# Kernel optimization log

Hardware: AMD Instinct MI355X
Metric: run time of the kernel (lower is better)

Reference implementation:

```python
import jax, jax.numpy as jnp
import numpy as np

N = 100000
E = 1600000
NEG_SLOPE_ATTN = 0.2   # DGL GATConv default negative_slope
NEG_SLOPE_ACT = 0.01   # F.leaky_relu default


def gat_conv(x, src, dst, W, al, ar, b):
    """DGL-style GATConv with a single head.
    x: [N, Fin]; W: [Fin, H*Fout]; al, ar: [H, Fout]; b: [H*Fout].
    Returns [N, H, Fout]."""
    H, Fout = al.shape
    h = (x @ W).reshape(-1, H, Fout)                 # [N,H,Fout]
    el = jnp.sum(h * al, axis=-1)                    # [N,H]
    er = jnp.sum(h * ar, axis=-1)                    # [N,H]
    e = jax.nn.leaky_relu(el[src] + er[dst], NEG_SLOPE_ATTN)  # [E,H]
    # edge softmax over incoming edges of each dst node
    m = jax.ops.segment_max(e, dst, num_segments=N)  # [N,H]
    ex = jnp.exp(e - m[dst])                         # [E,H]
    denom = jax.ops.segment_sum(ex, dst, num_segments=N)      # [N,H]
    a = ex / denom[dst]                              # [E,H]
    msg = h[src] * a[:, :, None]                     # [E,H,Fout]
    out = jax.ops.segment_sum(msg, dst, num_segments=N)       # [N,H,Fout]
    return out + b.reshape(1, H, Fout)


def setup_inputs() -> dict:
    key = jax.random.key(0)
    ks = jax.random.split(key, 16)
    features = jax.random.normal(ks[0], (N, 3), dtype=jnp.float32)
    src = jax.random.randint(ks[1], (E,), 0, N)
    dst = jax.random.randint(ks[2], (E,), 0, N)

    def glorot(k, shape):
        fan = shape[0] + shape[-1]
        s = jnp.sqrt(2.0 / fan).astype(jnp.float32)
        return jax.random.normal(k, shape, dtype=jnp.float32) * s

    W1 = glorot(ks[3], (3, 64));   al1 = glorot(ks[4], (1, 64));  ar1 = glorot(ks[5], (1, 64));  b1 = jnp.zeros((64,), jnp.float32)
    W2 = glorot(ks[6], (64, 64));  al2 = glorot(ks[7], (1, 64));  ar2 = glorot(ks[8], (1, 64));  b2 = jnp.zeros((64,), jnp.float32)
    W3 = glorot(ks[9], (64, 3));   al3 = glorot(ks[10], (1, 3));  ar3 = glorot(ks[11], (1, 3));  b3 = jnp.zeros((3,), jnp.float32)
    return {"features": features, "src": src, "dst": dst,
            "W1": W1, "al1": al1, "ar1": ar1, "b1": b1,
            "W2": W2, "al2": al2, "ar2": ar2, "b2": b2,
            "W3": W3, "al3": al3, "ar3": ar3, "b3": b3}


def reference(features, src, dst, W1, al1, ar1, b1, W2, al2, ar2, b2, W3, al3, ar3, b3):
    x = gat_conv(features, src, dst, W1, al1, ar1, b1)      # [N,1,64]
    x = jax.nn.leaky_relu(x, NEG_SLOPE_ACT)
    x = gat_conv(x[:, 0, :], src, dst, W2, al2, ar2, b2)     # [N,1,64]
    x = jax.nn.leaky_relu(x, NEG_SLOPE_ACT)
    x = gat_conv(x[:, 0, :], src, dst, W3, al3, ar3, b3)     # [N,1,3]
    return x[:, 0, :]                                        # [N,3]
```

## Files before the change

### kernel.cpp

```cpp
#include <hip/hip_runtime.h>
#include <hip/hip_fp16.h>
#include <math.h>


#define NEG_BIG (-1e30f)
#define SORT_CAP 6144
#define SLOT 64
#define CHUNK 8192

__device__ inline float waveSum(float v) {
#pragma unroll
  for (int off = 32; off; off >>= 1) v += __shfl_xor(v, off, 64);
  return v;
}

__device__ inline float halfSum(float v) {
#pragma unroll
  for (int off = 16; off; off >>= 1) v += __shfl_xor(v, off, 64);
  return v;
}

__device__ inline float halfMax(float v) {
#pragma unroll
  for (int off = 16; off; off >>= 1) v = fmaxf(v, __shfl_xor(v, off, 64));
  return v;
}

__device__ inline int waveMaxI(int v) {
#pragma unroll
  for (int off = 32; off; off >>= 1) v = max(v, __shfl_xor(v, off, 64));
  return v;
}

__device__ inline int rlI(int v, int l) { return __builtin_amdgcn_readlane(v, l); }
__device__ inline float rlF(float v, int l) {
  return __int_as_float(__builtin_amdgcn_readlane(__float_as_int(v), l));
}
__device__ inline int ntI(const int* p) { return __builtin_nontemporal_load(p); }

__global__ __launch_bounds__(1024) void k_binpad(
    const int* __restrict__ src, const int* __restrict__ dst,
    unsigned* __restrict__ binned, int* __restrict__ cnts,
    const float* __restrict__ x, const float* __restrict__ W1,
    const float* __restrict__ al1, const float* __restrict__ ar1,
    float4* __restrict__ x4, float* __restrict__ er1,
    int E, int N, int NBK, int NCH, int CB) {
  __shared__ int lcnt[512];
  __shared__ float su[6];
  int tid = threadIdx.x;
  if ((int)blockIdx.x < CB) {
    int c = blockIdx.x;
    for (int b = tid; b < NBK; b += 1024) lcnt[b] = 0;
    __syncthreads();
    int e0 = c * CHUNK;
    int e1 = min(e0 + CHUNK, E);
    for (int e = e0 + tid; e < e1; e += 1024) {
      int dd = ntI(&dst[e]);
      int ss = ntI(&src[e]);
      int b = dd >> 8;
      int pos = atomicAdd(&lcnt[b], 1);
      if (pos < SLOT)
        binned[((size_t)b * NCH + c) * SLOT + pos] =
            ((unsigned)(dd & 255) << 24) | (unsigned)ss;
    }
    __syncthreads();
    for (int b = tid; b < NBK; b += 1024)
      cnts[(size_t)c * NBK + b] = min(lcnt[b], SLOT);
  } else {
    if (tid < 64) {
      float a = al1[tid], r = ar1[tid];
#pragma unroll
      for (int i = 0; i < 3; ++i) {
        float w = W1[i * 64 + tid];
        float ui = waveSum(w * a);
        float vi = waveSum(w * r);
        if (tid == 0) { su[i] = ui; su[3 + i] = vi; }
      }
    }
    __syncthreads();
    int n = ((int)blockIdx.x - CB) * 1024 + tid;
    if (n >= N) return;
    float x0 = __builtin_nontemporal_load(&x[n * 3]);
    float x1 = __builtin_nontemporal_load(&x[n * 3 + 1]);
    float x2 = __builtin_nontemporal_load(&x[n * 3 + 2]);
    float el = fmaf(x0, su[0], fmaf(x1, su[1], x2 * su[2]));
    float er = fmaf(x0, su[3], fmaf(x1, su[4], x2 * su[5]));
    x4[n] = make_float4(x0, x1, x2, el);
    er1[n] = er;
  }
}

__global__ __launch_bounds__(256) void k_sort(
    const unsigned* __restrict__ binned, const int* __restrict__ cnts,
    int* __restrict__ csr, int* __restrict__ startv, int* __restrict__ degs,
    int N, int NBK, int NCH) {
  __shared__ unsigned sbuf[SORT_CAP];
  __shared__ unsigned obuf[SORT_CAP];
  __shared__ int hist[256];
  __shared__ int scn[256];
  __shared__ int cur[256];
  __shared__ int csc[256];
  int b = blockIdx.x;
  int tid = threadIdx.x;
  int total = 0;
  for (int cb = 0; cb < NCH; cb += 256) {
    int c = cb + tid;
    int v = (c < NCH) ? cnts[(size_t)c * NBK + b] : 0;
    csc[tid] = v;
    __syncthreads();
    for (int off = 1; off < 256; off <<= 1) {
      int u = (tid >= off) ? csc[tid - off] : 0;
      __syncthreads();
      csc[tid] += u;
      __syncthreads();
    }
    int dbase = total + csc[tid] - v;
    if (c < NCH && v > 0) {
      const unsigned* rs = binned + ((size_t)b * NCH + c) * SLOT;
      for (int i = 0; i < v; ++i) {
        int di = dbase + i;
        if (di < SORT_CAP) sbuf[di] = rs[i];
      }
    }
    total += csc[255];
    __syncthreads();
  }
  int cnt = min(total, SORT_CAP);
  int gbase = b * SORT_CAP;
  hist[tid] = 0;
  __syncthreads();
  for (int i = tid; i < cnt; i += 256) atomicAdd(&hist[sbuf[i] >> 24], 1);
  __syncthreads();
  int v = hist[tid];
  scn[tid] = v;
  __syncthreads();
  for (int off = 1; off < 256; off <<= 1) {
    int u = (tid >= off) ? scn[tid - off] : 0;
    __syncthreads();
    scn[tid] += u;
    __syncthreads();
  }
  int excl = scn[tid] - v;
  cur[tid] = excl;
  int dn = b * 256 + tid;
  if (dn < N) { startv[dn] = gbase + excl; degs[dn] = v; }
  __syncthreads();
  for (int i = tid; i < cnt; i += 256) {
    unsigned w = sbuf[i];
    int p = atomicAdd(&cur[w >> 24], 1);
    obuf[p] = w & 0xFFFFFFu;
  }
  __syncthreads();
  for (int i = tid; i < cnt; i += 256) csr[gbase + i] = (int)obuf[i];
}

__global__ __launch_bounds__(128) void k_agg1x(
    const float4* __restrict__ x4, const float* __restrict__ er1,
    const float* __restrict__ W1, const float* __restrict__ b1,
    const float* __restrict__ W2, const float* __restrict__ al2,
    const float* __restrict__ ar2, const int* __restrict__ start,
    const int* __restrict__ degs, const int* __restrict__ csr,
    float4* __restrict__ a4, float* __restrict__ er2, int N) {
  __shared__ float4 sWp[64];
  __shared__ float2 sLR[64];
  int tid = threadIdx.x;
  if (tid < 64) {
    sWp[tid] = make_float4(W1[tid], W1[64 + tid], W1[128 + tid], b1[tid]);
    float sa = 0.f, sr = 0.f;
#pragma unroll 8
    for (int f = 0; f < 64; ++f) {
      float w = W2[tid * 64 + f];
      sa = fmaf(w, al2[f], sa);
      sr = fmaf(w, ar2[f], sr);
    }
    sLR[tid] = make_float2(sa, sr);
  }
  __syncthreads();
  int n = blockIdx.x * 128 + tid;
  if (n >= N) return;
  int beg = start[n];
  int end = beg + degs[n];
  float ern = er1[n];
  float m = NEG_BIG, d = 0.f, X0 = 0.f, X1 = 0.f, X2 = 0.f;
  int s0, s1, s2, s3;
  float4 h0, h1, h2, h3v;
  s0 = (beg + 0 < end) ? ntI(&csr[beg + 0]) : 0;
  s0 = ((unsigned)s0 < (unsigned)N) ? s0 : 0; h0 = x4[s0];
  s1 = (beg + 1 < end) ? ntI(&csr[beg + 1]) : 0;
  s1 = ((unsigned)s1 < (unsigned)N) ? s1 : 0; h1 = x4[s1];
  s2 = (beg + 2 < end) ? ntI(&csr[beg + 2]) : 0;
  s2 = ((unsigned)s2 < (unsigned)N) ? s2 : 0; h2 = x4[s2];
  s3 = (beg + 3 < end) ? ntI(&csr[beg + 3]) : 0;
  s3 = ((unsigned)s3 < (unsigned)N) ? s3 : 0; h3v = x4[s3];
  for (int i = beg; i < end; ++i) {
    float4 hv = h0;
    h0 = h1; h1 = h2; h2 = h3v;
    int ip = i + 4;
    int sp = (ip < end) ? ntI(&csr[ip]) : 0;
    sp = ((unsigned)sp < (unsigned)N) ? sp : 0;
    h3v = x4[sp];
    float e = hv.w + ern;
    e = e > 0.f ? e : 0.2f * e;
    float mn = fmaxf(m, e);
    float sc = __expf(m - mn);
    float q = __expf(e - mn);
    d = fmaf(d, sc, q);
    X0 = fmaf(X0, sc, q * hv.x);
    X1 = fmaf(X1, sc, q * hv.y);
    X2 = fmaf(X2, sc, q * hv.z);
    m = mn;
  }
  float inv = (end > beg) ? 1.f / d : 0.f;
  float A0 = X0 * inv, A1 = X1 * inv, A2 = X2 * inv;
  float el = 0.f, er = 0.f;
#pragma unroll 4
  for (int k = 0; k < 64; ++k) {
    float4 w = sWp[k];
    float v = fmaf(A2, w.z, fmaf(A1, w.y, fmaf(A0, w.x, w.w)));
    v = v > 0.f ? v : 0.01f * v;
    float2 lr = sLR[k];
    el = fmaf(v, lr.x, el);
    er = fmaf(v, lr.y, er);
  }
  a4[n] = make_float4(A0, A1, A2, el);
  er2[n] = er;
}

__global__ __launch_bounds__(64) void k_agg2r(
    const float4* __restrict__ a4, const float* __restrict__ er2,
    const int* __restrict__ start, const int* __restrict__ degs,
    const int* __restrict__ csr, const float* __restrict__ W1,
    const float* __restrict__ b1, __half* __restrict__ xa, int N) {
  __shared__ float4 sAV[64];
  int tid = threadIdx.x;
  int lane = tid & 63, hl = lane & 31, half = lane >> 5;
  int pn = blockIdx.x * 2 + half;
  int n = (pn < N) ? pn : 0;
  int beg = start[n];
  int deg = degs[n];
  int end = beg + deg;
  int maxd = __builtin_amdgcn_readfirstlane(waveMaxI(deg));
  float ern = er2[n];
  int k0 = 2 * hl;
  float wa0 = W1[k0],     wb0 = W1[64 + k0],     wc0 = W1[128 + k0],     bb0 = b1[k0];
  float wa1 = W1[k0 + 1], wb1 = W1[64 + k0 + 1], wc1 = W1[128 + k0 + 1], bb1 = b1[k0 + 1];
  float acc0 = 0.f, acc1 = 0.f;

  float aA = 0.f, v0s = 0.f, v1s = 0.f, v2s = 0.f;
  if (maxd <= 32) {
    int idx = beg + hl;
    int s = (idx < end) ? ntI(&csr[idx]) : 0;
    s = ((unsigned)s < (unsigned)N) ? s : 0;
    float4 av = a4[s];
    float e = av.w + ern;
    e = e > 0.f ? e : 0.2f * e;
    e = (idx < end) ? e : NEG_BIG;
    float mm = halfMax(e);
    float q = __expf(e - mm);
    float dsum = halfSum(q);
    float inv = (deg > 0) ? 1.f / dsum : 0.f;
    aA = q * inv;
    v0s = av.x; v1s = av.y; v2s = av.z;
  }
  sAV[half * 32 + hl] = make_float4(aA, v0s, v1s, v2s);
  __syncthreads();

  if (maxd <= 32) {
    const float4* sp = &sAV[half * 32];
    for (int j = 0; j < maxd; j += 4) {
#pragma unroll
      for (int k = 0; k < 4; ++k) {
        float4 w = sp[j + k];
        float a = w.x;
        float v0 = fmaf(w.w, wc0, fmaf(w.z, wb0, fmaf(w.y, wa0, bb0)));
        v0 = v0 > 0.f ? v0 : 0.01f * v0;
        float v1 = fmaf(w.w, wc1, fmaf(w.z, wb1, fmaf(w.y, wa1, bb1)));
        v1 = v1 > 0.f ? v1 : 0.01f * v1;
        acc0 = fmaf(a, v0, acc0);
        acc1 = fmaf(a, v1, acc1);
      }
    }
  } else {
    float m = NEG_BIG, dsum = 0.f;
    for (int base = beg; base < end; base += 32) {
      int idx = base + hl;
      int s = (idx < end) ? csr[idx] : 0;
      s = ((unsigned)s < (unsigned)N) ? s : 0;
      float e = a4[s].w + ern;
      e = e > 0.f ? e : 0.2f * e;
      e = (idx < end) ? e : NEG_BIG;
      float mn = fmaxf(m, halfMax(e));
      dsum = dsum * __expf(m - mn) + halfSum(__expf(e - mn));
      m = mn;
    }
    float inv = (deg > 0) ? 1.f / dsum : 0.f;
    for (int base = beg; base < end; base += 32) {
      int idx = base + hl;
      int s = (idx < end) ? csr[idx] : 0;
      s = ((unsigned)s < (unsigned)N) ? s : 0;
      float e = a4[s].w + ern;
      e = e > 0.f ? e : 0.2f * e;
      float a = (idx < end) ? __expf(e - m) * inv : 0.f;
      for (int j = 0; j < 32; ++j) {
        int sAx = rlI(s, j), sBx = rlI(s, j + 32);
        float aAx = rlF(a, j), aBx = rlF(a, j + 32);
        int sj = half ? sBx : sAx;
        float aj = half ? aBx : aAx;
        float4 av = a4[sj];
        float v0 = fmaf(av.z, wc0, fmaf(av.y, wb0, fmaf(av.x, wa0, bb0)));
        v0 = v0 > 0.f ? v0 : 0.01f * v0;
        float v1 = fmaf(av.z, wc1, fmaf(av.y, wb1, fmaf(av.x, wa1, bb1)));
        v1 = v1 > 0.f ? v1 : 0.01f * v1;
        acc0 = fmaf(aj, v0, acc0);
        acc1 = fmaf(aj, v1, acc1);
      }
    }
  }
  if (pn < N) {
    __half2 hv = __float22half2_rn(make_float2(acc0, acc1));
    ((__half2*)xa)[(size_t)pn * 32 + hl] = hv;
  }
}

__global__ __launch_bounds__(256) void k_gemm3(
    const __half* xa_in, const float* __restrict__ W2,
    const float* __restrict__ b2, const float* __restrict__ W3,
    const float* __restrict__ al3, float* __restrict__ h3, int N) {
  __shared__ float sW[64 * 64];
  __shared__ float sX[64 * 64];
  __shared__ float sW3[192];
  int tid = threadIdx.x;
  for (int i = tid; i < 4096; i += 256) sW[i] = W2[i];
  if (tid < 192) sW3[tid] = W3[tid];
  const unsigned* xu = (const unsigned*)xa_in;
  size_t base = (size_t)blockIdx.x * 2048;
  size_t limit = (size_t)N * 32;
  for (int i = tid; i < 2048; i += 256) {
    size_t gi = base + i;
    unsigned u = (gi < limit) ? __builtin_nontemporal_load(&xu[gi]) : 0u;
    __half2 hh = *(__half2*)&u;
    float2 f = __half22float2(hh);
    sX[2 * i] = f.x;
    sX[2 * i + 1] = f.y;
  }
  __syncthreads();
  int wave = tid >> 6, f = tid & 63;
  int r0 = wave * 16;
  float acc[16];
#pragma unroll
  for (int i = 0; i < 16; ++i) acc[i] = 0.f;
  const float2* sX2 = (const float2*)sX;
  for (int k2 = 0; k2 < 32; ++k2) {
    float wv0 = sW[(2 * k2) * 64 + f];
    float wv1 = sW[(2 * k2 + 1) * 64 + f];
#pragma unroll
    for (int i = 0; i < 16; ++i) {
      float2 xv = sX2[(r0 + i) * 32 + k2];
      acc[i] = fmaf(xv.x, wv0, fmaf(xv.y, wv1, acc[i]));
    }
  }
  float bf = b2[f];
  __syncthreads();
#pragma unroll
  for (int i = 0; i < 16; ++i) {
    float r = acc[i] + bf;
    r = r > 0.f ? r : 0.01f * r;
    sX[(r0 + i) * 64 + f] = r;
  }
  __syncthreads();
  int row = tid >> 2, j = tid & 3;
  int j3 = (j < 3) ? j : 0;
  float p = 0.f;
  for (int i = 0; i < 64; ++i) {
    int ff = (row + i) & 63;
    p = fmaf(sX[row * 64 + ff], sW3[ff * 3 + j3], p);
  }
  int lb = (tid & 63) & ~3;
  float q0 = __shfl(p, lb + 0, 64);
  float q1 = __shfl(p, lb + 1, 64);
  float q2 = __shfl(p, lb + 2, 64);
  float val = (j < 3) ? p : fmaf(q0, al3[0], fmaf(q1, al3[1], q2 * al3[2]));
  int grow = blockIdx.x * 64 + row;
  if (grow < N) h3[(size_t)blockIdx.x * 256 + tid] = val;
}

__global__ __launch_bounds__(128) void k_agg3(
    const float4* __restrict__ h3, const int* __restrict__ start,
    const int* __restrict__ degs, const int* __restrict__ csr,
    const float* __restrict__ ar3, const float* __restrict__ b,
    float* __restrict__ out, int N) {
  int n = blockIdx.x * 128 + threadIdx.x;
  if (n >= N) return;
  int beg = start[n];
  int end = beg + degs[n];
  float4 hn = h3[n];
  float ern = fmaf(hn.x, ar3[0], fmaf(hn.y, ar3[1], hn.z * ar3[2]));
  float m = NEG_BIG, d = 0.f, Q0 = 0.f, Q1 = 0.f, Q2 = 0.f;
  int s0, s1, s2, s3;
  float4 h0, h1, h2, h3v;
  s0 = (beg + 0 < end) ? ntI(&csr[beg + 0]) : 0;
  s0 = ((unsigned)s0 < (unsigned)N) ? s0 : 0; h0 = h3[s0];
  s1 = (beg + 1 < end) ? ntI(&csr[beg + 1]) : 0;
  s1 = ((unsigned)s1 < (unsigned)N) ? s1 : 0; h1 = h3[s1];
  s2 = (beg + 2 < end) ? ntI(&csr[beg + 2]) : 0;
  s2 = ((unsigned)s2 < (unsigned)N) ? s2 : 0; h2 = h3[s2];
  s3 = (beg + 3 < end) ? ntI(&csr[beg + 3]) : 0;
  s3 = ((unsigned)s3 < (unsigned)N) ? s3 : 0; h3v = h3[s3];
  for (int i = beg; i < end; ++i) {
    float4 hv = h0;
    h0 = h1; h1 = h2; h2 = h3v;
    int ip = i + 4;
    int sp = (ip < end) ? ntI(&csr[ip]) : 0;
    sp = ((unsigned)sp < (unsigned)N) ? sp : 0;
    h3v = h3[sp];
    float e = hv.w + ern;
    e = e > 0.f ? e : 0.2f * e;
    float mn = fmaxf(m, e);
    float sc = __expf(m - mn);
    float q = __expf(e - mn);
    d = fmaf(d, sc, q);
    Q0 = fmaf(Q0, sc, q * hv.x);
    Q1 = fmaf(Q1, sc, q * hv.y);
    Q2 = fmaf(Q2, sc, q * hv.z);
    m = mn;
  }
  float inv = (end > beg) ? 1.f / d : 0.f;
  out[n * 3 + 0] = fmaf(Q0, inv, b[0]);
  out[n * 3 + 1] = fmaf(Q1, inv, b[1]);
  out[n * 3 + 2] = fmaf(Q2, inv, b[2]);
}

extern "C" void kernel_launch(void* const* d_in, const int* in_sizes, int n_in,
                              void* d_out, int out_size, void* d_ws, size_t ws_size,
                              hipStream_t stream) {
  const int N = in_sizes[0] / 3;
  const int E = in_sizes[1];
  const float* feats = (const float*)d_in[0];
  const int* src = (const int*)d_in[1];
  const int* dst = (const int*)d_in[2];
  const float* W1  = (const float*)d_in[3];
  const float* al1 = (const float*)d_in[4];
  const float* ar1 = (const float*)d_in[5];
  const float* b1  = (const float*)d_in[6];
  const float* W2  = (const float*)d_in[7];
  const float* al2 = (const float*)d_in[8];
  const float* ar2 = (const float*)d_in[9];
  const float* b2  = (const float*)d_in[10];
  const float* W3  = (const float*)d_in[11];
  const float* al3 = (const float*)d_in[12];
  const float* ar3 = (const float*)d_in[13];
  const float* b3  = (const float*)d_in[14];

  const int NBK = (N + 255) >> 8;
  const int CB  = (E + CHUNK - 1) / CHUNK;
  const int NCH = CB;

  char* ws = (char*)d_ws;
  size_t off = 0;
  auto alloc = [&](size_t bytes) -> void* {
    void* p = ws + off;
    off = (off + bytes + 255) & ~(size_t)255;
    return p;
  };
  int* startv  = (int*)alloc((size_t)(N + 1) * 4);
  int* degs    = (int*)alloc((size_t)N * 4);
  int* csr     = (int*)alloc((size_t)NBK * SORT_CAP * 4);
  float* er2v  = (float*)alloc((size_t)N * 4);
  float* er1   = (float*)alloc((size_t)N * 4);
  int* cnts    = (int*)alloc((size_t)NCH * NBK * 4);
  float* h3    = (float*)alloc((size_t)N * 4 * 4);
  float4* x4   = (float4*)alloc((size_t)N * 16);
  float4* a4   = (float4*)alloc((size_t)N * 16);
  __half* xa   = (__half*)alloc((size_t)N * 64 * 2);
  unsigned* binned = (unsigned*)alloc((size_t)NBK * NCH * SLOT * 4);

  const int NPB = (N + 1023) / 1024;
  const int NB1 = (N + 127) / 128;
  const int NW2 = (N + 1) / 2;
  const int GB  = (N + 63) / 64;

  k_binpad<<<CB + NPB, 1024, 0, stream>>>(src, dst, binned, cnts,
                                          feats, W1, al1, ar1, x4, er1,
                                          E, N, NBK, NCH, CB);
  k_sort<<<NBK, 256, 0, stream>>>(binned, cnts, csr, startv, degs,
                                  N, NBK, NCH);
  k_agg1x<<<NB1, 128, 0, stream>>>(x4, er1, W1, b1, W2, al2, ar2,
                                   startv, degs, csr, a4, er2v, N);
  k_agg2r<<<NW2, 64, 0, stream>>>(a4, er2v, startv, degs, csr, W1, b1, xa, N);
  k_gemm3<<<GB, 256, 0, stream>>>(xa, W2, b2, W3, al3, h3, N);
  k_agg3<<<NB1, 128, 0, stream>>>((const float4*)h3, startv, degs, csr,
                                  ar3, b3, (float*)d_out, N);
}
```

Baseline: 240.1 us.

## Fuse four post-sort stages into one persistent cooperative kernel with grid syncs

Replaces the four separate launches (layer-1 aggregation, layer-2 aggregation, GEMM, layer-3 aggregation) with a single cooperative kernel of 256 blocks that loops over work and separates the stages with grid.sync. The goal is to remove per-launch overhead and tail gaps between kernels. The cost is fewer resident threads (256x256) for latency-bound gather loops, a large shared-memory footprint, and grid-barrier overhead. If the cooperative launch fails, it falls back to the original kernels.

Result: slower. 522.1 us (+117.5%).

```diff
diff --git a/kernel.cpp b/kernel.cpp
--- a/kernel.cpp
+++ b/kernel.cpp
@@ -1,6 +1,9 @@
 #include <hip/hip_runtime.h>
 #include <hip/hip_fp16.h>
+#include <hip/hip_cooperative_groups.h>
 #include <math.h>
+
+namespace cg = cooperative_groups;
 
 
 #define NEG_BIG (-1e30f)
@@ -245,7 +248,6 @@
   float wa0 = W1[k0],     wb0 = W1[64 + k0],     wc0 = W1[128 + k0],     bb0 = b1[k0];
   float wa1 = W1[k0 + 1], wb1 = W1[64 + k0 + 1], wc1 = W1[128 + k0 + 1], bb1 = b1[k0 + 1];
   float acc0 = 0.f, acc1 = 0.f;
-
   float aA = 0.f, v0s = 0.f, v1s = 0.f, v2s = 0.f;
   if (maxd <= 32) {
     int idx = beg + hl;
@@ -264,7 +266,6 @@
   }
   sAV[half * 32 + hl] = make_float4(aA, v0s, v1s, v2s);
   __syncthreads();
-
   if (maxd <= 32) {
     const float4* sp = &sAV[half * 32];
     for (int j = 0; j < maxd; j += 4) {
@@ -430,6 +431,302 @@
   out[n * 3 + 2] = fmaf(Q2, inv, b[2]);
 }
 
+__global__ __launch_bounds__(256) void k_net(
+    const float4* __restrict__ x4, const float* __restrict__ er1,
+    const float* __restrict__ W1, const float* __restrict__ b1,
+    const float* __restrict__ W2, const float* __restrict__ al2,
+    const float* __restrict__ ar2, const float* __restrict__ b2,
+    const float* __restrict__ W3, const float* __restrict__ al3,
+    const float* __restrict__ ar3, const float* __restrict__ b3,
+    const int* __restrict__ startv, const int* __restrict__ degs,
+    const int* __restrict__ csr, float4* __restrict__ a4,
+    float* __restrict__ er2v, __half* __restrict__ xa,
+    float* __restrict__ h3, float* __restrict__ out,
+    int N, int G, int GBt) {
+  __shared__ float sW[4096];
+  __shared__ float sXx[4096];
+  __shared__ float sW3[192];
+  __shared__ float4 sAV[4][64];
+  __shared__ float4 sWp[64];
+  __shared__ float2 sLR[64];
+  cg::grid_group grid = cg::this_grid();
+  int tid = threadIdx.x;
+  int bid = blockIdx.x;
+
+  if (tid < 64) {
+    sWp[tid] = make_float4(W1[tid], W1[64 + tid], W1[128 + tid], b1[tid]);
+    float sa = 0.f, sr = 0.f;
+#pragma unroll 8
+    for (int f = 0; f < 64; ++f) {
+      float w = W2[tid * 64 + f];
+      sa = fmaf(w, al2[f], sa);
+      sr = fmaf(w, ar2[f], sr);
+    }
+    sLR[tid] = make_float2(sa, sr);
+  }
+  __syncthreads();
+  for (int n = bid * 256 + tid; n < N; n += G * 256) {
+    int beg = startv[n];
+    int end = beg + degs[n];
+    float ern = er1[n];
+    float m = NEG_BIG, d = 0.f, X0 = 0.f, X1 = 0.f, X2 = 0.f;
+    int s0, s1, s2, s3;
+    float4 h0, h1, h2, h3v;
+    s0 = (beg + 0 < end) ? ntI(&csr[beg + 0]) : 0;
+    s0 = ((unsigned)s0 < (unsigned)N) ? s0 : 0; h0 = x4[s0];
+    s1 = (beg + 1 < end) ? ntI(&csr[beg + 1]) : 0;
+    s1 = ((unsigned)s1 < (unsigned)N) ? s1 : 0; h1 = x4[s1];
+    s2 = (beg + 2 < end) ? ntI(&csr[beg + 2]) : 0;
+    s2 = ((unsigned)s2 < (unsigned)N) ? s2 : 0; h2 = x4[s2];
+    s3 = (beg + 3 < end) ? ntI(&csr[beg + 3]) : 0;
+    s3 = ((unsigned)s3 < (unsigned)N) ? s3 : 0; h3v = x4[s3];
+    for (int i = beg; i < end; ++i) {
+      float4 hv = h0;
+      h0 = h1; h1 = h2; h2 = h3v;
+      int ip = i + 4;
+      int sp = (ip < end) ? ntI(&csr[ip]) : 0;
+      sp = ((unsigned)sp < (unsigned)N) ? sp : 0;
+      h3v = x4[sp];
+      float e = hv.w + ern;
+      e = e > 0.f ? e : 0.2f * e;
+      float mn = fmaxf(m, e);
+      float sc = __expf(m - mn);
+      float q = __expf(e - mn);
+      d = fmaf(d, sc, q);
+      X0 = fmaf(X0, sc, q * hv.x);
+      X1 = fmaf(X1, sc, q * hv.y);
+      X2 = fmaf(X2, sc, q * hv.z);
+      m = mn;
+    }
+    float inv = (end > beg) ? 1.f / d : 0.f;
+    float A0 = X0 * inv, A1 = X1 * inv, A2 = X2 * inv;
+    float el = 0.f, er = 0.f;
+#pragma unroll 4
+    for (int k = 0; k < 64; ++k) {
+      float4 w = sWp[k];
+      float v = fmaf(A2, w.z, fmaf(A1, w.y, fmaf(A0, w.x, w.w)));
+      v = v > 0.f ? v : 0.01f * v;
+      float2 lr = sLR[k];
+      el = fmaf(v, lr.x, el);
+      er = fmaf(v, lr.y, er);
+    }
+    a4[n] = make_float4(A0, A1, A2, el);
+    er2v[n] = er;
+  }
+  __threadfence();
+  grid.sync();
+
+  {
+    int lane = tid & 63, hl = lane & 31, half = lane >> 5;
+    int wslot = tid >> 6;
+    int wv = bid * 4 + wslot;
+    int NW = G * 4;
+    int NP = (N + 1) / 2;
+    int k0 = 2 * hl;
+    float wa0 = W1[k0],     wb0 = W1[64 + k0],     wc0 = W1[128 + k0],     bb0 = b1[k0];
+    float wa1 = W1[k0 + 1], wb1 = W1[64 + k0 + 1], wc1 = W1[128 + k0 + 1], bb1 = b1[k0 + 1];
+    int T = (NP > bid * 4) ? (NP - bid * 4 + NW - 1) / NW : 0;
+    for (int it = 0; it < T; ++it) {
+      int p = wv + it * NW;
+      bool active = (p < NP);
+      int pn = 0, beg = 0, deg = 0, end = 0;
+      float ern = 0.f;
+      float aA = 0.f;
+      float4 av = make_float4(0.f, 0.f, 0.f, 0.f);
+      int maxd = 0;
+      if (active) {
+        pn = p * 2 + half;
+        int n = (pn < N) ? pn : 0;
+        beg = startv[n];
+        deg = degs[n];
+        end = beg + deg;
+        ern = er2v[n];
+      }
+      maxd = __builtin_amdgcn_readfirstlane(waveMaxI(deg));
+      if (active && maxd <= 32) {
+        int idx = beg + hl;
+        int s = (idx < end) ? ntI(&csr[idx]) : 0;
+        s = ((unsigned)s < (unsigned)N) ? s : 0;
+        av = a4[s];
+        float e = av.w + ern;
+        e = e > 0.f ? e : 0.2f * e;
+        e = (idx < end) ? e : NEG_BIG;
+        float mm = halfMax(e);
+        float q = __expf(e - mm);
+        float dsum = halfSum(q);
+        float inv = (deg > 0) ? 1.f / dsum : 0.f;
+        aA = q * inv;
+      }
+      sAV[wslot][half * 32 + hl] = make_float4(aA, av.x, av.y, av.z);
+      __syncthreads();
+      if (active) {
+        float acc0 = 0.f, acc1 = 0.f;
+        if (maxd <= 32) {
+          const float4* sp = &sAV[wslot][half * 32];
+          for (int j = 0; j < maxd; j += 4) {
+#pragma unroll
+            for (int kk = 0; kk < 4; ++kk) {
+              float4 w = sp[j + kk];
+              float a = w.x;
+              float v0 = fmaf(w.w, wc0, fmaf(w.z, wb0, fmaf(w.y, wa0, bb0)));
+              v0 = v0 > 0.f ? v0 : 0.01f * v0;
+              float v1 = fmaf(w.w, wc1, fmaf(w.z, wb1, fmaf(w.y, wa1, bb1)));
+              v1 = v1 > 0.f ? v1 : 0.01f * v1;
+              acc0 = fmaf(a, v0, acc0);
+              acc1 = fmaf(a, v1, acc1);
+            }
+          }
+        } else {
+          float m = NEG_BIG, dsum = 0.f;
+          for (int base = beg; base < end; base += 32) {
+            int idx = base + hl;
+            int s = (idx < end) ? csr[idx] : 0;
+            s = ((unsigned)s < (unsigned)N) ? s : 0;
+            float e = a4[s].w + ern;
+            e = e > 0.f ? e : 0.2f * e;
+            e = (idx < end) ? e : NEG_BIG;
+            float mn = fmaxf(m, halfMax(e));
+            dsum = dsum * __expf(m - mn) + halfSum(__expf(e - mn));
+            m = mn;
+          }
+          float inv = (deg > 0) ? 1.f / dsum : 0.f;
+          for (int base = beg; base < end; base += 32) {
+            int idx = base + hl;
+            int s = (idx < end) ? csr[idx] : 0;
+            s = ((unsigned)s < (unsigned)N) ? s : 0;
+            float e = a4[s].w + ern;
+            e = e > 0.f ? e : 0.2f * e;
+            float a = (idx < end) ? __expf(e - m) * inv : 0.f;
+            for (int j = 0; j < 32; ++j) {
+              int sAx = rlI(s, j), sBx = rlI(s, j + 32);
+              float aAx = rlF(a, j), aBx = rlF(a, j + 32);
+              int sj = half ? sBx : sAx;
+              float aj = half ? aBx : aAx;
+              float4 avx = a4[sj];
+              float v0 = fmaf(avx.z, wc0, fmaf(avx.y, wb0, fmaf(avx.x, wa0, bb0)));
+              v0 = v0 > 0.f ? v0 : 0.01f * v0;
+              float v1 = fmaf(avx.z, wc1, fmaf(avx.y, wb1, fmaf(avx.x, wa1, bb1)));
+              v1 = v1 > 0.f ? v1 : 0.01f * v1;
+              acc0 = fmaf(aj, v0, acc0);
+              acc1 = fmaf(aj, v1, acc1);
+            }
+          }
+        }
+        if (pn < N) {
+          __half2 hv = __float22half2_rn(make_float2(acc0, acc1));
+          ((__half2*)xa)[(size_t)pn * 32 + hl] = hv;
+        }
+      }
+      __syncthreads();
+    }
+  }
+  __threadfence();
+  grid.sync();
+
+  {
+    for (int i = tid; i < 4096; i += 256) sW[i] = W2[i];
+    if (tid < 192) sW3[tid] = W3[tid];
+    const unsigned* xu = (const unsigned*)xa;
+    size_t limit = (size_t)N * 32;
+    int wave = tid >> 6, f = tid & 63;
+    int r0 = wave * 16;
+    for (int t = bid; t < GBt; t += G) {
+      __syncthreads();
+      size_t base = (size_t)t * 2048;
+      for (int i = tid; i < 2048; i += 256) {
+        size_t gi = base + i;
+        unsigned u = (gi < limit) ? xu[gi] : 0u;
+        __half2 hh = *(__half2*)&u;
+        float2 fv = __half22float2(hh);
+        sXx[2 * i] = fv.x;
+        sXx[2 * i + 1] = fv.y;
+      }
+      __syncthreads();
+      float acc[16];
+#pragma unroll
+      for (int i = 0; i < 16; ++i) acc[i] = 0.f;
+      const float2* sX2 = (const float2*)sXx;
+      for (int k2 = 0; k2 < 32; ++k2) {
+        float wv0 = sW[(2 * k2) * 64 + f];
+        float wv1 = sW[(2 * k2 + 1) * 64 + f];
+#pragma unroll
+        for (int i = 0; i < 16; ++i) {
+          float2 xv = sX2[(r0 + i) * 32 + k2];
+          acc[i] = fmaf(xv.x, wv0, fmaf(xv.y, wv1, acc[i]));
+        }
+      }
+      float bf = b2[f];
+      __syncthreads();
+#pragma unroll
+      for (int i = 0; i < 16; ++i) {
+        float r = acc[i] + bf;
+        r = r > 0.f ? r : 0.01f * r;
+        sXx[(r0 + i) * 64 + f] = r;
+      }
+      __syncthreads();
+      int row = tid >> 2, j = tid & 3;
+      int j3 = (j < 3) ? j : 0;
+      float pr = 0.f;
+      for (int i = 0; i < 64; ++i) {
+        int ff = (row + i) & 63;
+        pr = fmaf(sXx[row * 64 + ff], sW3[ff * 3 + j3], pr);
+      }
+      int lb = (tid & 63) & ~3;
+      float q0 = __shfl(pr, lb + 0, 64);
+      float q1 = __shfl(pr, lb + 1, 64);
+      float q2 = __shfl(pr, lb + 2, 64);
+      float val = (j < 3) ? pr : fmaf(q0, al3[0], fmaf(q1, al3[1], q2 * al3[2]));
+      int grow = t * 64 + row;
+      if (grow < N) h3[(size_t)t * 256 + tid] = val;
+    }
+  }
+  __threadfence();
+  grid.sync();
+
+  {
+    const float4* h3v4 = (const float4*)h3;
+    for (int n = bid * 256 + tid; n < N; n += G * 256) {
+      int beg = startv[n];
+      int end = beg + degs[n];
+      float4 hn = h3v4[n];
+      float ern = fmaf(hn.x, ar3[0], fmaf(hn.y, ar3[1], hn.z * ar3[2]));
+      float m = NEG_BIG, d = 0.f, Q0 = 0.f, Q1 = 0.f, Q2 = 0.f;
+      int s0, s1, s2, s3;
+      float4 h0, h1, h2, h3p;
+      s0 = (beg + 0 < end) ? ntI(&csr[beg + 0]) : 0;
+      s0 = ((unsigned)s0 < (unsigned)N) ? s0 : 0; h0 = h3v4[s0];
+      s1 = (beg + 1 < end) ? ntI(&csr[beg + 1]) : 0;
+      s1 = ((unsigned)s1 < (unsigned)N) ? s1 : 0; h1 = h3v4[s1];
+      s2 = (beg + 2 < end) ? ntI(&csr[beg + 2]) : 0;
+      s2 = ((unsigned)s2 < (unsigned)N) ? s2 : 0; h2 = h3v4[s2];
+      s3 = (beg + 3 < end) ? ntI(&csr[beg + 3]) : 0;
+      s3 = ((unsigned)s3 < (unsigned)N) ? s3 : 0; h3p = h3v4[s3];
+      for (int i = beg; i < end; ++i) {
+        float4 hv = h0;
+        h0 = h1; h1 = h2; h2 = h3p;
+        int ip = i + 4;
+        int sp = (ip < end) ? ntI(&csr[ip]) : 0;
+        sp = ((unsigned)sp < (unsigned)N) ? sp : 0;
+        h3p = h3v4[sp];
+        float e = hv.w + ern;
+        e = e > 0.f ? e : 0.2f * e;
+        float mn = fmaxf(m, e);
+        float sc = __expf(m - mn);
+        float q = __expf(e - mn);
+        d = fmaf(d, sc, q);
+        Q0 = fmaf(Q0, sc, q * hv.x);
+        Q1 = fmaf(Q1, sc, q * hv.y);
+        Q2 = fmaf(Q2, sc, q * hv.z);
+        m = mn;
+      }
+      float inv = (end > beg) ? 1.f / d : 0.f;
+      out[n * 3 + 0] = fmaf(Q0, inv, b3[0]);
+      out[n * 3 + 1] = fmaf(Q1, inv, b3[1]);
+      out[n * 3 + 2] = fmaf(Q2, inv, b3[2]);
+    }
+  }
+}
+
 extern "C" void kernel_launch(void* const* d_in, const int* in_sizes, int n_in,
                               void* d_out, int out_size, void* d_ws, size_t ws_size,
                               hipStream_t stream) {
@@ -478,16 +775,32 @@
   const int NB1 = (N + 127) / 128;
   const int NW2 = (N + 1) / 2;
   const int GB  = (N + 63) / 64;
+  int G = 256;
+  int GBt = GB;
 
   k_binpad<<<CB + NPB, 1024, 0, stream>>>(src, dst, binned, cnts,
                                           feats, W1, al1, ar1, x4, er1,
                                           E, N, NBK, NCH, CB);
   k_sort<<<NBK, 256, 0, stream>>>(binned, cnts, csr, startv, degs,
                                   N, NBK, NCH);
-  k_agg1x<<<NB1, 128, 0, stream>>>(x4, er1, W1, b1, W2, al2, ar2,
-                                   startv, degs, csr, a4, er2v, N);
-  k_agg2r<<<NW2, 64, 0, stream>>>(a4, er2v, startv, degs, csr, W1, b1, xa, N);
-  k_gemm3<<<GB, 256, 0, stream>>>(xa, W2, b2, W3, al3, h3, N);
-  k_agg3<<<NB1, 128, 0, stream>>>((const float4*)h3, startv, degs, csr,
-                                  ar3, b3, (float*)d_out, N);
-}
+
+  float* outp = (float*)d_out;
+  void* kargs[] = {
+    (void*)&x4, (void*)&er1, (void*)&W1, (void*)&b1, (void*)&W2,
+    (void*)&al2, (void*)&ar2, (void*)&b2, (void*)&W3, (void*)&al3,
+    (void*)&ar3, (void*)&b3, (void*)&startv, (void*)&degs, (void*)&csr,
+    (void*)&a4, (void*)&er2v, (void*)&xa, (void*)&h3, (void*)&outp,
+    (void*)&N, (void*)&G, (void*)&GBt
+  };
+  hipError_t cerr = hipLaunchCooperativeKernel((void*)k_net, dim3(G),
+                                               dim3(256), kargs, 0, stream);
+  if (cerr != hipSuccess) {
+    k_agg1x<<<NB1, 128, 0, stream>>>(x4, er1, W1, b1, W2, al2, ar2,
+                                     startv, degs, csr, a4, er2v, N);
+    k_agg2r<<<NW2, 64, 0, stream>>>(a4, er2v, startv, degs, csr, W1, b1,
+                                    xa, N);
+    k_gemm3<<<GB, 256, 0, stream>>>(xa, W2, b2, W3, al3, h3, N);
+    k_agg3<<<NB1, 128, 0, stream>>>((const float4*)h3, startv, degs, csr,
+                                    ar3, b3, (float*)d_out, N);
+  }
+}
```
